# Optimization experiments

Hardware: AMD Instinct MI355X
Metric: run time of the kernel (lower is better)

## Reference

```python
import jax, jax.numpy as jnp
import numpy as np

N_EMBD = 1024
N_HEAD = 16
HEAD_DIM = N_EMBD // N_HEAD


def setup_inputs() -> dict:
    key = jax.random.key(0)
    ks = jax.random.split(key, 9)
    B, T, C = 4, 2048, N_EMBD
    s = 1.0 / np.sqrt(C)
    return {
        "x": jax.random.normal(ks[0], (B, T, C), dtype=jnp.float32),
        "Wq": jax.random.normal(ks[1], (C, C), dtype=jnp.float32) * s,
        "bq": jnp.zeros((C,), dtype=jnp.float32),
        "Wk": jax.random.normal(ks[2], (C, C), dtype=jnp.float32) * s,
        "bk": jnp.zeros((C,), dtype=jnp.float32),
        "Wv": jax.random.normal(ks[3], (C, C), dtype=jnp.float32) * s,
        "bv": jnp.zeros((C,), dtype=jnp.float32),
        "Wo": jax.random.normal(ks[4], (C, C), dtype=jnp.float32) * s,
        "bo": jnp.zeros((C,), dtype=jnp.float32),
    }


def reference(x, Wq, bq, Wk, bk, Wv, bv, Wo, bo):
    B, T, C = x.shape
    H, D = N_HEAD, HEAD_DIM
    # torch Linear: y = x @ W.T + b ; here W stored as (in, out) so y = x @ W + b
    q = (x @ Wq + bq).reshape(B, T, H, D).transpose(0, 2, 1, 3)  # [B,H,T,D]
    k = (x @ Wk + bk).reshape(B, T, H, D).transpose(0, 2, 1, 3)
    v = (x @ Wv + bv).reshape(B, T, H, D).transpose(0, 2, 1, 3)
    scores = jnp.einsum('bhqd,bhkd->bhqk', q, k) / jnp.sqrt(jnp.float32(D))
    causal = jnp.tril(jnp.ones((T, T), dtype=bool))  # [T,T]
    scores = jnp.where(causal[None, None, :, :], scores, -jnp.inf)
    weights = jax.nn.softmax(scores, axis=-1)
    # dropout disabled (eval mode / deterministic reference)
    out = jnp.einsum('bhqk,bhkd->bhqd', weights, v)  # [B,H,T,D]
    out = out.transpose(0, 2, 1, 3).reshape(B, T, C)
    return out @ Wo + bo
```

## Files before the change

### kernel.cpp

```cpp
#include <hip/hip_runtime.h>
#include <stdint.h>
#include <stddef.h>

#define NB 4
#define NT 2048
#define NC 1024
#define NH 16
#define ND 64
#define NM (NB*NT)

typedef __bf16 bf16_t;
typedef __attribute__((ext_vector_type(8)))  __bf16 bf16x8;
typedef __attribute__((ext_vector_type(4)))  __bf16 bf16x4;
typedef __attribute__((ext_vector_type(2)))  __bf16 bf16x2;
typedef __attribute__((ext_vector_type(4)))  float  f32x4;
typedef __attribute__((ext_vector_type(16))) float  f32x16;
typedef __attribute__((ext_vector_type(4)))  unsigned int u32x4;

#define QK_SCALE_LOG2E 0.18033688011112042f

__device__ __forceinline__ f32x4 mfma_bf16(bf16x8 a, bf16x8 b, f32x4 c) {
  return __builtin_amdgcn_mfma_f32_16x16x32_bf16(a, b, c, 0, 0, 0);
}
__device__ __forceinline__ f32x16 mfma32(bf16x8 a, bf16x8 b, f32x16 c) {
  return __builtin_amdgcn_mfma_f32_32x32x16_bf16(a, b, c, 0, 0, 0);
}

__device__ __forceinline__ void gld_lds16(const void* g, void* l) {
  __builtin_amdgcn_global_load_lds(
      (const __attribute__((address_space(1))) void*)g,
      (__attribute__((address_space(3))) void*)l, 16, 0, 0);
}

__device__ __forceinline__ unsigned int pack_bf16(float a, float b) {
  bf16x2 t; t[0] = (bf16_t)a; t[1] = (bf16_t)b;
  return __builtin_bit_cast(unsigned int, t);
}

#if __has_builtin(__builtin_amdgcn_permlane32_swap)
typedef __attribute__((ext_vector_type(2))) unsigned int u32x2;
__device__ __forceinline__ void plswap(unsigned int &a, unsigned int &b) {
  u32x2 r = __builtin_amdgcn_permlane32_swap(a, b, false, false);
  a = r[0]; b = r[1];
}
#else
__device__ __forceinline__ void plswap(unsigned int &a, unsigned int &b) {
  asm volatile("s_nop 1\n\tv_permlane32_swap_b32 %0, %1\n\ts_nop 1"
               : "+v"(a), "+v"(b));
}
#endif

__global__ __launch_bounds__(256) void cast_x_kernel(const float* __restrict__ x,
                                                     bf16_t* __restrict__ xb, int n4) {
  const int stride = gridDim.x * blockDim.x;
  for (int i = blockIdx.x * blockDim.x + threadIdx.x; i < n4; i += stride) {
    float4 v = reinterpret_cast<const float4*>(x)[i];
    bf16x4 o;
    o[0] = (bf16_t)v.x; o[1] = (bf16_t)v.y; o[2] = (bf16_t)v.z; o[3] = (bf16_t)v.w;
    reinterpret_cast<bf16x4*>(xb)[i] = o;
  }
}

__global__ __launch_bounds__(256) void wtrans_kernel(
    const float* __restrict__ Wq, const float* __restrict__ Wk,
    const float* __restrict__ Wv, const float* __restrict__ Wo,
    bf16_t* __restrict__ Tq, bf16_t* __restrict__ Tk,
    bf16_t* __restrict__ Tv, bf16_t* __restrict__ To) {
  __shared__ float tile[32][33];
  const int wsel = blockIdx.x >> 10;
  const float* W = (wsel == 0) ? Wq : (wsel == 1) ? Wk : (wsel == 2) ? Wv : Wo;
  bf16_t*     WT = (wsel == 0) ? Tq : (wsel == 1) ? Tk : (wsel == 2) ? Tv : To;
  const int blk = blockIdx.x & 1023;
  const int t = threadIdx.x;
  const int tx = t & 31, ty = t >> 5;
  const int k0 = (blk & 31) << 5;
  const int n0 = (blk >> 5) << 5;
#pragma unroll
  for (int i = 0; i < 4; ++i)
    tile[ty + 8*i][tx] = W[(size_t)(k0 + ty + 8*i)*NC + n0 + tx];
  __syncthreads();
#pragma unroll
  for (int i = 0; i < 4; ++i)
    WT[(size_t)(n0 + ty + 8*i)*NC + k0 + tx] = (bf16_t)tile[tx][ty + 8*i];
}

__global__ __launch_bounds__(256) void vtrans_kernel(const bf16_t* __restrict__ v,
                                                     bf16_t* __restrict__ vt) {
  __shared__ bf16_t tile[64][72];
  const int tid = threadIdx.x;
  const int bh = blockIdx.x >> 5;
  const int t0 = (blockIdx.x & 31) << 6;
  const size_t base = (size_t)bh * (NT * ND);
  {
    const int r = tid >> 2, dc = (tid & 3) << 4;
    const bf16_t* src = v + base + (size_t)(t0 + r)*ND + dc;
    const bf16x8 a = *reinterpret_cast<const bf16x8*>(src);
    const bf16x8 b = *reinterpret_cast<const bf16x8*>(src + 8);
    *reinterpret_cast<bf16x8*>(&tile[r][dc])     = a;
    *reinterpret_cast<bf16x8*>(&tile[r][dc + 8]) = b;
  }
  __syncthreads();
  {
    const int d = tid >> 2, tc = (tid & 3) << 4;
    bf16x8 a, b;
#pragma unroll
    for (int i = 0; i < 8; ++i) { a[i] = tile[tc + i][d]; b[i] = tile[tc + 8 + i][d]; }
    bf16_t* dst = vt + base + (size_t)d*NT + t0 + tc;
    *reinterpret_cast<bf16x8*>(dst)     = a;
    *reinterpret_cast<bf16x8*>(dst + 8) = b;
  }
}

template<int MODE>
__global__ __launch_bounds__(256) void gemm_bt_kernel(
    const bf16_t* __restrict__ A, const bf16_t* __restrict__ BT,
    int M, int N, int K,
    bf16_t* __restrict__ qo, bf16_t* __restrict__ ko, bf16_t* __restrict__ vo,
    const float* __restrict__ b0, const float* __restrict__ b1, const float* __restrict__ b2,
    float* __restrict__ outp, const float* __restrict__ bo)
{
  const int lane = threadIdx.x & 63;
  const int wv = threadIdx.x >> 6;
  const int wr = wv >> 1, wc = wv & 1;
  const int l15 = lane & 15, lg = lane >> 4;
  const int nbn = N >> 7;
  const int bm = blockIdx.x / nbn, bn = blockIdx.x % nbn;
  const int m0 = bm << 7, n0 = bn << 7;

  __shared__ char smem[32768];
  char* As = smem;
  char* Bs = smem + 16384;

  f32x4 acc[4][4] = {};

  const int nkt = K >> 6;
  for (int kt = 0; kt < nkt; ++kt) {
    const int k0 = kt << 6;
    __syncthreads();
#pragma unroll
    for (int i = 0; i < 4; ++i) {
      const int seg = i*4 + wv;
      const int lin = seg*64 + lane;
      const int row = lin >> 3;
      const int ch  = (lin & 7) ^ (row & 7);
      gld_lds16(A  + (size_t)(m0 + row)*K + k0 + (ch << 3), As + seg*1024);
      gld_lds16(BT + (size_t)(n0 + row)*K + k0 + (ch << 3), Bs + seg*1024);
    }
    __syncthreads();
#pragma unroll
    for (int ks = 0; ks < 2; ++ks) {
      bf16x8 af[4], bfr[4];
#pragma unroll
      for (int fr = 0; fr < 4; ++fr) {
        const int row = wr*64 + fr*16 + l15;
        const int ch  = (ks*4 + lg) ^ (row & 7);
        af[fr] = *reinterpret_cast<const bf16x8*>(As + row*128 + ch*16);
      }
#pragma unroll
      for (int fc = 0; fc < 4; ++fc) {
        const int row = wc*64 + fc*16 + l15;
        const int ch  = (ks*4 + lg) ^ (row & 7);
        bfr[fc] = *reinterpret_cast<const bf16x8*>(Bs + row*128 + ch*16);
      }
#pragma unroll
      for (int fr = 0; fr < 4; ++fr)
#pragma unroll
        for (int fc = 0; fc < 4; ++fc)
          acc[fr][fc] = mfma_bf16(af[fr], bfr[fc], acc[fr][fc]);
    }
  }

#pragma unroll
  for (int fr = 0; fr < 4; ++fr) {
#pragma unroll
    for (int fc = 0; fc < 4; ++fc) {
      const int mrow0 = m0 + wr*64 + fr*16 + (lg << 2);
      const int ncol  = n0 + wc*64 + fc*16 + l15;
      if (MODE == 0) {
        const int mat = ncol >> 10, c = ncol & 1023;
        const int h = c >> 6, d = c & 63;
        bf16_t* dst = (mat == 0) ? qo : ((mat == 1) ? ko : vo);
        const float* bptr = (mat == 0) ? b0 : ((mat == 1) ? b1 : b2);
        const float bias = bptr[c];
        const float scl = (mat == 0) ? QK_SCALE_LOG2E : 1.0f;
#pragma unroll
        for (int r = 0; r < 4; ++r) {
          const int mm = mrow0 + r;
          const int bb = mm >> 11, tt = mm & (NT - 1);
          dst[((((size_t)bb*NH + h)*NT + tt) << 6) + d] =
              (bf16_t)((acc[fr][fc][r] + bias) * scl);
        }
      } else {
        const float bias = bo[ncol];
#pragma unroll
        for (int r = 0; r < 4; ++r)
          outp[(size_t)(mrow0 + r)*N + ncol] = acc[fr][fc][r] + bias;
      }
    }
  }
}

__global__ __launch_bounds__(256, 2) void attn_kernel(
    const bf16_t* __restrict__ q, const bf16_t* __restrict__ k, const bf16_t* __restrict__ vt,
    bf16_t* __restrict__ o)
{
  const int tid  = threadIdx.x;
  const int lane = tid & 63;
  const int wv   = tid >> 6;
  const int l31  = lane & 31, h = lane >> 5;

  const int tpair = blockIdx.x >> 6;
  const int bh    = blockIdx.x & 63;
  const int bb = bh >> 4, hh = bh & 15;

  __shared__ char smem[65536];
  char* const ks0 = smem;
  char* const ks1 = smem + 16384;
  char* const vs0 = smem + 32768;
  char* const vs1 = smem + 49152;

  const size_t base = (size_t)bh * (NT * ND);
  const bf16_t* Kg = k  + base;
  const bf16_t* Vg = vt + base;

  int offk[4], offv[4], segb[4];
#pragma unroll
  for (int p = 0; p < 4; ++p) {
    const int c = p*256 + tid;
    const int krow = c >> 3;
    const int kch  = (c & 7) ^ (krow & 7);
    offk[p] = krow*ND + (kch << 3);
    const int vrow = c >> 4;
    const int vdc  = (c & 15) ^ (vrow & 15);
    offv[p] = vrow*NT + (vdc << 3);
    segb[p] = (p*4 + wv) << 10;
  }

  bf16x8 ones8;
#pragma unroll
  for (int jj2 = 0; jj2 < 8; ++jj2) ones8[jj2] = (bf16_t)1.0f;

#pragma unroll
  for (int p = 0; p < 4; ++p) {
    gld_lds16(Kg + offk[p], ks0 + segb[p]);
    gld_lds16(Vg + offv[p], vs0 + segb[p]);
  }

  int jj = 0;

#pragma unroll 1
  for (int pass = 0; pass < 2; ++pass) {
    const int tile = (pass == 0) ? tpair : 15 - tpair;
    const int q0   = tile << 7;
    const int q0w  = q0 + wv*32;
    const int qg   = q0w + l31;

    bf16x8 qf[4];
    {
      const bf16_t* Qg = q + base + (size_t)qg*ND + 8*h;
#pragma unroll
      for (int ds = 0; ds < 4; ++ds)
        qf[ds] = *reinterpret_cast<const bf16x8*>(Qg + 16*ds);
    }

    f32x16 oc[2] = {};
    f32x16 lacc = {};

    const int nkv = tile + 1;

#pragma unroll 1
    for (int j = 0; j < nkv; ++j, ++jj) {
      const bool cur1 = (jj & 1) != 0;
      char* const Kc = cur1 ? ks1 : ks0;
      char* const Vc = cur1 ? vs1 : vs0;

      asm volatile("s_waitcnt vmcnt(0)" ::: "memory");
      __builtin_amdgcn_s_barrier();
      __builtin_amdgcn_sched_barrier(0);

      int nj = (j + 1 < nkv) ? (j + 1) : ((pass == 0) ? 0 : -1);
      if (nj >= 0) {
        char* const Kn = cur1 ? ks0 : ks1;
        char* const Vn = cur1 ? vs0 : vs1;
        const bf16_t* kp = Kg + (size_t)nj*(128*ND);
        const bf16_t* vp = Vg + (size_t)nj*128;
#pragma unroll
        for (int p = 0; p < 4; ++p) {
          gld_lds16(kp + offk[p], Kn + segb[p]);
          gld_lds16(vp + offv[p], Vn + segb[p]);
        }
        __builtin_amdgcn_sched_barrier(0);
      }

      const int ktile0 = j << 7;
#pragma unroll 1
      for (int hf = 0; hf < 2; ++hf) {
        const int kb0 = ktile0 + (hf << 6);
        if (kb0 > q0w + 31) break;

        f32x16 st[2] = {};
        __builtin_amdgcn_s_setprio(1);
#pragma unroll
        for (int ds = 0; ds < 4; ++ds) {
#pragma unroll
          for (int kt = 0; kt < 2; ++kt) {
            const int row = (hf*2 + kt)*32 + l31;
            const int cl  = (2*ds + h) ^ (row & 7);
            const bf16x8 kfr = *reinterpret_cast<const bf16x8*>(Kc + row*128 + cl*16);
            st[kt] = mfma32(kfr, qf[ds], st[kt]);
          }
        }
        __builtin_amdgcn_s_setprio(0);

        if (kb0 + 63 > q0w) {
          const int qrel = qg - kb0 - 4*h;
#pragma unroll
          for (int kt = 0; kt < 2; ++kt)
#pragma unroll
            for (int r = 0; r < 16; ++r) {
              const int kc = (r & 3) + 8*(r >> 2) + 32*kt;
              st[kt][r] = (kc > qrel) ? 0.0f : exp2f(st[kt][r]);
            }
        } else {
#pragma unroll
          for (int kt = 0; kt < 2; ++kt)
#pragma unroll
            for (int r = 0; r < 16; ++r)
              st[kt][r] = exp2f(st[kt][r]);
        }

#pragma unroll
        for (int kt = 0; kt < 2; ++kt) {
#pragma unroll
          for (int g = 0; g < 2; ++g) {
            unsigned int wa = pack_bf16(st[kt][8*g + 0], st[kt][8*g + 1]);
            unsigned int wb = pack_bf16(st[kt][8*g + 2], st[kt][8*g + 3]);
            unsigned int wc = pack_bf16(st[kt][8*g + 4], st[kt][8*g + 5]);
            unsigned int wd = pack_bf16(st[kt][8*g + 6], st[kt][8*g + 7]);
            plswap(wa, wc);
            plswap(wb, wd);
            u32x4 pb; pb[0] = wa; pb[1] = wb; pb[2] = wc; pb[3] = wd;
            const bf16x8 pf = __builtin_bit_cast(bf16x8, pb);
            const int cv = 2*(4*hf + 2*kt + g) + h;
            __builtin_amdgcn_s_setprio(1);
            lacc = mfma32(ones8, pf, lacc);
#pragma unroll
            for (int da = 0; da < 2; ++da) {
              const int row = 32*da + l31;
              const int lcv = cv ^ (row & 15);
              const bf16x8 vf = *reinterpret_cast<const bf16x8*>(Vc + row*256 + lcv*16);
              oc[da] = mfma32(vf, pf, oc[da]);
            }
            __builtin_amdgcn_s_setprio(0);
          }
        }
      }
    }

    const float rl = 1.0f / lacc[0];
    bf16_t* orow = o + ((size_t)bb*NT + qg)*NC + hh*ND;
#pragma unroll
    for (int da = 0; da < 2; ++da) {
#pragma unroll
      for (int u = 0; u < 4; ++u) {
        bf16x4 ov;
#pragma unroll
        for (int jj3 = 0; jj3 < 4; ++jj3) ov[jj3] = (bf16_t)(oc[da][4*u + jj3] * rl);
        *reinterpret_cast<bf16x4*>(orow + 32*da + 8*u + 4*h) = ov;
      }
    }
  }
}

extern "C" void kernel_launch(void* const* d_in, const int* in_sizes, int n_in,
                              void* d_out, int out_size, void* d_ws, size_t ws_size,
                              hipStream_t stream) {
  (void)in_sizes; (void)n_in; (void)out_size;
  const float* x  = (const float*)d_in[0];
  const float* Wq = (const float*)d_in[1];
  const float* bq = (const float*)d_in[2];
  const float* Wk = (const float*)d_in[3];
  const float* bk = (const float*)d_in[4];
  const float* Wv = (const float*)d_in[5];
  const float* bv = (const float*)d_in[6];
  const float* Wo = (const float*)d_in[7];
  const float* bo = (const float*)d_in[8];
  float* out = (float*)d_out;

  const size_t off_xb    = 0;
  const size_t off_wqkvT = 16777216;
  const size_t off_woT   = 23068672;
  const size_t off_q     = 25165824;
  const size_t off_k     = 41943040;
  const size_t off_v     = 58720256;
  const size_t off_attn  = 75497472;
  const size_t need      = 92274688;
  if (ws_size < need) return;

  char* ws = (char*)d_ws;
  bf16_t* xb    = (bf16_t*)(ws + off_xb);
  bf16_t* wqkvT = (bf16_t*)(ws + off_wqkvT);
  bf16_t* woT   = (bf16_t*)(ws + off_woT);
  bf16_t* qb    = (bf16_t*)(ws + off_q);
  bf16_t* kb    = (bf16_t*)(ws + off_k);
  bf16_t* vb    = (bf16_t*)(ws + off_v);
  bf16_t* vtb   = (bf16_t*)(ws + off_xb);
  bf16_t* attnb = (bf16_t*)(ws + off_attn);

  cast_x_kernel<<<dim3(2048), dim3(256), 0, stream>>>(x, xb, NM*NC/4);
  wtrans_kernel<<<dim3(4096), dim3(256), 0, stream>>>(
      Wq, Wk, Wv, Wo, wqkvT, wqkvT + 1048576, wqkvT + 2097152, woT);

  gemm_bt_kernel<0><<<dim3(64*24), dim3(256), 0, stream>>>(
      xb, wqkvT, NM, 3*NC, NC, qb, kb, vb, bq, bk, bv, nullptr, nullptr);

  vtrans_kernel<<<dim3(2048), dim3(256), 0, stream>>>(vb, vtb);

  attn_kernel<<<dim3(8*64), dim3(256), 0, stream>>>(qb, kb, vtb, attnb);

  gemm_bt_kernel<1><<<dim3(64*8), dim3(256), 0, stream>>>(
      attnb, woT, NM, NC, NC, nullptr, nullptr, nullptr, nullptr, nullptr, nullptr,
      out, bo);
}
```

Before: 178.7 us.

## Double-buffer GEMM with 256x128 tiles, 512 threads, and XCD-aware block swizzle

Rewrites the projection GEMM to use 256x128 block tiles with 8 waves, double-buffered LDS staging that prefetches the next K tile while the current one is computed, precomputed load offsets, s_setprio around MFMA bursts, and a block-index swizzle that groups tiles per XCD. The aim is to hide global-to-LDS latency, drop one barrier per K step, and improve L2 locality. The cost is 96KB of LDS per block, which limits residency, and fewer blocks for the output projection (256), which may underfill the GPU.

```diff
diff --git a/kernel.cpp b/kernel.cpp
--- a/kernel.cpp
+++ b/kernel.cpp
@@ -112,41 +112,77 @@
 }
 
 template<int MODE>
-__global__ __launch_bounds__(256) void gemm_bt_kernel(
+__global__ __launch_bounds__(512, 2) void gemm_bt256_kernel(
     const bf16_t* __restrict__ A, const bf16_t* __restrict__ BT,
     int M, int N, int K,
     bf16_t* __restrict__ qo, bf16_t* __restrict__ ko, bf16_t* __restrict__ vo,
     const float* __restrict__ b0, const float* __restrict__ b1, const float* __restrict__ b2,
     float* __restrict__ outp, const float* __restrict__ bo)
 {
-  const int lane = threadIdx.x & 63;
-  const int wv = threadIdx.x >> 6;
-  const int wr = wv >> 1, wc = wv & 1;
-  const int l15 = lane & 15, lg = lane >> 4;
+  const int tid  = threadIdx.x;
+  const int lane = tid & 63;
+  const int wv   = tid >> 6;
+  const int wr   = wv >> 1, wc = wv & 1;
+  const int l15  = lane & 15, lg = lane >> 4;
+
   const int nbn = N >> 7;
-  const int bm = blockIdx.x / nbn, bn = blockIdx.x % nbn;
-  const int m0 = bm << 7, n0 = bn << 7;
-
-  __shared__ char smem[32768];
-  char* As = smem;
-  char* Bs = smem + 16384;
+  const int cpx = gridDim.x >> 3;
+  const int swz = (blockIdx.x & 7)*cpx + (blockIdx.x >> 3);
+  const int bm = swz / nbn, bn = swz % nbn;
+  const int m0 = bm << 8, n0 = bn << 7;
+
+  __shared__ char smem[98304];
 
   f32x4 acc[4][4] = {};
 
+  int offa[4], offb[2];
+#pragma unroll
+  for (int p = 0; p < 4; ++p) {
+    const int c = p*512 + tid;
+    const int row = c >> 3, ch = (c & 7) ^ (row & 7);
+    offa[p] = row*K + (ch << 3);
+  }
+#pragma unroll
+  for (int p = 0; p < 2; ++p) {
+    const int c = p*512 + tid;
+    const int row = c >> 3, ch = (c & 7) ^ (row & 7);
+    offb[p] = row*K + (ch << 3);
+  }
+  const int sega = wv << 10;
+
+  const bf16_t* Ab = A  + (size_t)m0 * K;
+  const bf16_t* Bb = BT + (size_t)n0 * K;
+
   const int nkt = K >> 6;
+
+  {
+    char* const As = smem;
+    char* const Bs = smem + 32768;
+#pragma unroll
+    for (int p = 0; p < 4; ++p) gld_lds16(Ab + offa[p], As + p*8192 + sega);
+#pragma unroll
+    for (int p = 0; p < 2; ++p) gld_lds16(Bb + offb[p], Bs + p*8192 + sega);
+  }
+
   for (int kt = 0; kt < nkt; ++kt) {
-    const int k0 = kt << 6;
-    __syncthreads();
-#pragma unroll
-    for (int i = 0; i < 4; ++i) {
-      const int seg = i*4 + wv;
-      const int lin = seg*64 + lane;
-      const int row = lin >> 3;
-      const int ch  = (lin & 7) ^ (row & 7);
-      gld_lds16(A  + (size_t)(m0 + row)*K + k0 + (ch << 3), As + seg*1024);
-      gld_lds16(BT + (size_t)(n0 + row)*K + k0 + (ch << 3), Bs + seg*1024);
-    }
-    __syncthreads();
+    char* const As = smem + (kt & 1)*49152;
+    char* const Bs = As + 32768;
+
+    asm volatile("s_waitcnt vmcnt(0)" ::: "memory");
+    __builtin_amdgcn_s_barrier();
+    __builtin_amdgcn_sched_barrier(0);
+
+    if (kt + 1 < nkt) {
+      char* const An = smem + ((kt + 1) & 1)*49152;
+      char* const Bn = An + 32768;
+      const int k0 = (kt + 1) << 6;
+#pragma unroll
+      for (int p = 0; p < 4; ++p) gld_lds16(Ab + k0 + offa[p], An + p*8192 + sega);
+#pragma unroll
+      for (int p = 0; p < 2; ++p) gld_lds16(Bb + k0 + offb[p], Bn + p*8192 + sega);
+      __builtin_amdgcn_sched_barrier(0);
+    }
+
 #pragma unroll
     for (int ks = 0; ks < 2; ++ks) {
       bf16x8 af[4], bfr[4];
@@ -162,11 +198,13 @@
         const int ch  = (ks*4 + lg) ^ (row & 7);
         bfr[fc] = *reinterpret_cast<const bf16x8*>(Bs + row*128 + ch*16);
       }
+      __builtin_amdgcn_s_setprio(1);
 #pragma unroll
       for (int fr = 0; fr < 4; ++fr)
 #pragma unroll
         for (int fc = 0; fc < 4; ++fc)
           acc[fr][fc] = mfma_bf16(af[fr], bfr[fc], acc[fr][fc]);
+      __builtin_amdgcn_s_setprio(0);
     }
   }
 
@@ -411,14 +449,14 @@
   wtrans_kernel<<<dim3(4096), dim3(256), 0, stream>>>(
       Wq, Wk, Wv, Wo, wqkvT, wqkvT + 1048576, wqkvT + 2097152, woT);
 
-  gemm_bt_kernel<0><<<dim3(64*24), dim3(256), 0, stream>>>(
+  gemm_bt256_kernel<0><<<dim3(768), dim3(512), 0, stream>>>(
       xb, wqkvT, NM, 3*NC, NC, qb, kb, vb, bq, bk, bv, nullptr, nullptr);
 
   vtrans_kernel<<<dim3(2048), dim3(256), 0, stream>>>(vb, vtb);
 
   attn_kernel<<<dim3(8*64), dim3(256), 0, stream>>>(qb, kb, vtb, attnb);
 
-  gemm_bt_kernel<1><<<dim3(64*8), dim3(256), 0, stream>>>(
+  gemm_bt256_kernel<1><<<dim3(256), dim3(512), 0, stream>>>(
       attnb, woT, NM, NC, NC, nullptr, nullptr, nullptr, nullptr, nullptr, nullptr,
       out, bo);
 }
```

Result: faster. 168.7 us (-5.6%).
